# Kernel tuning notes

Measured on AMD Instinct MI355X. Metric: run time of the kernel, lower is better.

## Reference

```python
import jax, jax.numpy as jnp
import numpy as np

T = 0.1          # temperature from CLloss.__init__
PD_EPS = 1e-6    # nn.PairwiseDistance default eps (added to the difference)
NORM_EPS = 1e-12 # F.normalize eps


def setup_inputs() -> dict:
    key = jax.random.key(0)
    k1, k2 = jax.random.split(key)
    embed = jax.random.normal(k1, (16384, 2048), dtype=jnp.float32)
    labels = jax.random.randint(k2, (16384, 20), 0, 2, dtype=jnp.int32)
    return {"embed": embed, "labels": labels}


def reference(embed, labels):
    lab = labels.astype(jnp.float32)
    n = embed.shape[0]
    # F.normalize(embed, dim=-1): x / max(||x||, eps)
    norm = jnp.maximum(jnp.linalg.norm(embed, axis=-1, keepdims=True), NORM_EPS)
    e = embed / norm
    # NOTE: original torch code has `return loss` inside the outer loop, so only
    # anchor i=0 contributes. Faithfully reproduce that.
    # pairwise distance: ||e0 - ej + eps||_2 for j = 1..n-1
    d = jnp.linalg.norm(e[0] - e[1:] + PD_EPS, axis=-1)            # [n-1]
    log_sim = -d / T                                               # log exp(-d/t)
    c = jnp.dot(lab[1:], lab[0])                                   # [n-1] label overlap counts
    Ci = 1e-12 + jnp.sum(c)
    Ei = 1e-12 + jnp.sum(jnp.exp(log_sim))
    # Li = sum_j -(c_j/Ci) * log(exp(-d_j/t)/Ei)
    Li = jnp.sum(-(c / Ci) * (log_sim - jnp.log(Ei)))
    return Li / n
```

## Files before the change

### kernel.cpp

```cpp
#include <hip/hip_runtime.h>
#include <math.h>

#define NROW 16384
#define DIM 2048
#define NLAB 20
#define T_INV 10.0f
#define PD_EPS 1e-6f
#define NORM_EPS 1e-12f

#define BLOCKS 2048
#define THREADS 256
#define WPB (THREADS / 64)
#define TOTAL_WAVES (BLOCKS * WPB)
#define FRAG 8


__global__ __launch_bounds__(THREADS) void clloss_main(const float* __restrict__ embed,
                                                       const int* __restrict__ labels,
                                                       float4* __restrict__ partials) {
    const int tid = threadIdx.x;
    const int lane = tid & 63;
    const int wid = tid >> 6;

    const float4* row0 = (const float4*)embed;
    float4 v[FRAG];
#pragma unroll
    for (int it = 0; it < FRAG; ++it) v[it] = row0[it * 64 + lane];

    float s = 0.f;
#pragma unroll
    for (int it = 0; it < FRAG; ++it)
        s += v[it].x * v[it].x + v[it].y * v[it].y + v[it].z * v[it].z + v[it].w * v[it].w;
    for (int o = 32; o; o >>= 1) s += __shfl_xor(s, o, 64);
    const float inv0 = 1.0f / fmaxf(sqrtf(s), NORM_EPS);

    float4 av[FRAG];
    float saa = 0.f;
#pragma unroll
    for (int it = 0; it < FRAG; ++it) {
        av[it].x = v[it].x * inv0 + PD_EPS;
        av[it].y = v[it].y * inv0 + PD_EPS;
        av[it].z = v[it].z * inv0 + PD_EPS;
        av[it].w = v[it].w * inv0 + PD_EPS;
        saa += av[it].x * av[it].x + av[it].y * av[it].y +
               av[it].z * av[it].z + av[it].w * av[it].w;
    }
    for (int o = 32; o; o >>= 1) saa += __shfl_xor(saa, o, 64);
    const float S_aa = saa;

    const float lab0 = (lane < NLAB) ? (float)labels[lane] : 0.f;

    const int gw = blockIdx.x * WPB + wid;
    float acc_e = 0.f, acc_c = 0.f, acc_cl = 0.f;

    for (int row = 1 + gw; row < NROW; row += TOTAL_WAVES) {
        const float4* b4 = (const float4*)(embed + (size_t)row * DIM);
        float sab = 0.f, sbb = 0.f;
#pragma unroll
        for (int it = 0; it < FRAG; ++it) {
            float4 b = b4[it * 64 + lane];
            sab += av[it].x * b.x + av[it].y * b.y + av[it].z * b.z + av[it].w * b.w;
            sbb += b.x * b.x + b.y * b.y + b.z * b.z + b.w * b.w;
        }
        float c = (lane < NLAB) ? lab0 * (float)labels[row * NLAB + lane] : 0.f;

        for (int o = 32; o; o >>= 1) {
            sab += __shfl_xor(sab, o, 64);
            sbb += __shfl_xor(sbb, o, 64);
            c   += __shfl_xor(c,   o, 64);
        }
        float invb = 1.0f / fmaxf(sqrtf(sbb), NORM_EPS);
        float d2 = fmaxf(S_aa + invb * (invb * sbb - 2.0f * sab), 0.f);
        float ls = -sqrtf(d2) * T_INV;
        acc_e  += expf(ls);
        acc_c  += c;
        acc_cl += c * ls;
    }

    __shared__ float wsum[WPB][3];
    if (lane == 0) {
        wsum[wid][0] = acc_e;
        wsum[wid][1] = acc_c;
        wsum[wid][2] = acc_cl;
    }
    __syncthreads();
    if (tid == 0) {
        float4 p;
        p.x = wsum[0][0] + wsum[1][0] + wsum[2][0] + wsum[3][0];
        p.y = wsum[0][1] + wsum[1][1] + wsum[2][1] + wsum[3][1];
        p.z = wsum[0][2] + wsum[1][2] + wsum[2][2] + wsum[3][2];
        p.w = 0.f;
        partials[blockIdx.x] = p;
    }
}

__global__ __launch_bounds__(THREADS) void clloss_final(const float4* __restrict__ partials,
                                                        float* __restrict__ out) {
    __shared__ float red[THREADS / 64][3];
    const int tid = threadIdx.x;
    const int lane = tid & 63, wid = tid >> 6;

    float se = 0.f, sc = 0.f, scl = 0.f;
    for (int i = tid; i < BLOCKS; i += THREADS) {
        float4 p = partials[i];
        se += p.x; sc += p.y; scl += p.z;
    }
    for (int o = 32; o; o >>= 1) {
        se  += __shfl_xor(se,  o, 64);
        sc  += __shfl_xor(sc,  o, 64);
        scl += __shfl_xor(scl, o, 64);
    }
    if (lane == 0) { red[wid][0] = se; red[wid][1] = sc; red[wid][2] = scl; }
    __syncthreads();
    if (tid == 0) {
        se = sc = scl = 0.f;
        for (int w = 0; w < THREADS / 64; ++w) {
            se += red[w][0]; sc += red[w][1]; scl += red[w][2];
        }
        float Ci = 1e-12f + sc;
        float Ei = 1e-12f + se;
        float Li = (sc * logf(Ei) - scl) / Ci;
        out[0] = Li / (float)NROW;
    }
}

extern "C" void kernel_launch(void* const* d_in, const int* in_sizes, int n_in,
                              void* d_out, int out_size, void* d_ws, size_t ws_size,
                              hipStream_t stream) {
    const float* embed = (const float*)d_in[0];
    const int* labels = (const int*)d_in[1];
    float* out = (float*)d_out;
    float4* partials = (float4*)d_ws;

    clloss_main<<<BLOCKS, THREADS, 0, stream>>>(embed, labels, partials);
    clloss_final<<<1, THREADS, 0, stream>>>(partials, out);
}
```

Measured before the change: 194.7 us.

## Software-pipeline row loads with register double-buffering and fewer blocks

Each wave now prefetches the next row it owns into a second register buffer while it computes on the current row, so load latency overlaps the reduction math. The grid shrinks from 2048 to 512 blocks, which gives each wave about eight rows instead of two so the prefetch has something to overlap, and it also cuts the number of partials the final kernel has to sum. The anchor self-norm is now derived algebraically from its raw sum and sum of squares, which removes one extra wave reduction. In exchange, register use doubles for the row buffers and fewer waves are in flight to hide memory latency.

```diff
diff --git a/kernel.cpp b/kernel.cpp
--- a/kernel.cpp
+++ b/kernel.cpp
@@ -8,7 +8,7 @@
 #define PD_EPS 1e-6f
 #define NORM_EPS 1e-12f
 
-#define BLOCKS 2048
+#define BLOCKS 512
 #define THREADS 256
 #define WPB (THREADS / 64)
 #define TOTAL_WAVES (BLOCKS * WPB)
@@ -23,58 +23,78 @@
     const int wid = tid >> 6;
 
     const float4* row0 = (const float4*)embed;
-    float4 v[FRAG];
+    float4 a[FRAG];
 #pragma unroll
-    for (int it = 0; it < FRAG; ++it) v[it] = row0[it * 64 + lane];
+    for (int it = 0; it < FRAG; ++it) a[it] = row0[it * 64 + lane];
 
-    float s = 0.f;
-#pragma unroll
-    for (int it = 0; it < FRAG; ++it)
-        s += v[it].x * v[it].x + v[it].y * v[it].y + v[it].z * v[it].z + v[it].w * v[it].w;
-    for (int o = 32; o; o >>= 1) s += __shfl_xor(s, o, 64);
-    const float inv0 = 1.0f / fmaxf(sqrtf(s), NORM_EPS);
-
-    float4 av[FRAG];
-    float saa = 0.f;
+    float s = 0.f, sx = 0.f;
 #pragma unroll
     for (int it = 0; it < FRAG; ++it) {
-        av[it].x = v[it].x * inv0 + PD_EPS;
-        av[it].y = v[it].y * inv0 + PD_EPS;
-        av[it].z = v[it].z * inv0 + PD_EPS;
-        av[it].w = v[it].w * inv0 + PD_EPS;
-        saa += av[it].x * av[it].x + av[it].y * av[it].y +
-               av[it].z * av[it].z + av[it].w * av[it].w;
+        s  += a[it].x * a[it].x + a[it].y * a[it].y + a[it].z * a[it].z + a[it].w * a[it].w;
+        sx += a[it].x + a[it].y + a[it].z + a[it].w;
     }
-    for (int o = 32; o; o >>= 1) saa += __shfl_xor(saa, o, 64);
-    const float S_aa = saa;
-
+    for (int o = 32; o; o >>= 1) {
+        s  += __shfl_xor(s,  o, 64);
+        sx += __shfl_xor(sx, o, 64);
+    }
+    const float inv0 = 1.0f / fmaxf(sqrtf(s), NORM_EPS);
+    const float S_aa = inv0 * inv0 * s + 2.0f * PD_EPS * inv0 * sx
+                     + (float)DIM * PD_EPS * PD_EPS;
+#pragma unroll
+    for (int it = 0; it < FRAG; ++it) {
+        a[it].x = a[it].x * inv0 + PD_EPS;
+        a[it].y = a[it].y * inv0 + PD_EPS;
+        a[it].z = a[it].z * inv0 + PD_EPS;
+        a[it].w = a[it].w * inv0 + PD_EPS;
+    }
     const float lab0 = (lane < NLAB) ? (float)labels[lane] : 0.f;
 
     const int gw = blockIdx.x * WPB + wid;
     float acc_e = 0.f, acc_c = 0.f, acc_cl = 0.f;
 
-    for (int row = 1 + gw; row < NROW; row += TOTAL_WAVES) {
-        const float4* b4 = (const float4*)(embed + (size_t)row * DIM);
+    int row = 1 + gw;
+    float4 cur[FRAG], nxt[FRAG];
+    {
+        const float4* p = (const float4*)(embed + (size_t)row * DIM);
+#pragma unroll
+        for (int it = 0; it < FRAG; ++it) cur[it] = p[it * 64 + lane];
+    }
+
+    while (row < NROW) {
+        const int rnext = row + TOTAL_WAVES;
+        const bool has_next = rnext < NROW;
+        if (has_next) {
+            const float4* q = (const float4*)(embed + (size_t)rnext * DIM);
+#pragma unroll
+            for (int it = 0; it < FRAG; ++it) nxt[it] = q[it * 64 + lane];
+        }
+        float c = (lane < NLAB) ? lab0 * (float)labels[row * NLAB + lane] : 0.f;
+
         float sab = 0.f, sbb = 0.f;
 #pragma unroll
         for (int it = 0; it < FRAG; ++it) {
-            float4 b = b4[it * 64 + lane];
-            sab += av[it].x * b.x + av[it].y * b.y + av[it].z * b.z + av[it].w * b.w;
-            sbb += b.x * b.x + b.y * b.y + b.z * b.z + b.w * b.w;
+            sab += a[it].x * cur[it].x + a[it].y * cur[it].y
+                 + a[it].z * cur[it].z + a[it].w * cur[it].w;
+            sbb += cur[it].x * cur[it].x + cur[it].y * cur[it].y
+                 + cur[it].z * cur[it].z + cur[it].w * cur[it].w;
         }
-        float c = (lane < NLAB) ? lab0 * (float)labels[row * NLAB + lane] : 0.f;
-
         for (int o = 32; o; o >>= 1) {
             sab += __shfl_xor(sab, o, 64);
             sbb += __shfl_xor(sbb, o, 64);
             c   += __shfl_xor(c,   o, 64);
         }
-        float invb = 1.0f / fmaxf(sqrtf(sbb), NORM_EPS);
-        float d2 = fmaxf(S_aa + invb * (invb * sbb - 2.0f * sab), 0.f);
-        float ls = -sqrtf(d2) * T_INV;
+        const float invb = 1.0f / fmaxf(sqrtf(sbb), NORM_EPS);
+        const float d2 = fmaxf(S_aa + invb * (invb * sbb - 2.0f * sab), 0.f);
+        const float ls = -sqrtf(d2) * T_INV;
         acc_e  += expf(ls);
         acc_c  += c;
         acc_cl += c * ls;
+
+        if (has_next) {
+#pragma unroll
+            for (int it = 0; it < FRAG; ++it) cur[it] = nxt[it];
+        }
+        row = rnext;
     }
 
     __shared__ float wsum[WPB][3];
```

After: 191.1 us. Within noise of the previous version (-1.9%).
